# Performance work log

Hardware: AMD Instinct MI355X
Metric: run time of the kernel (lower is better)

Reference implementation:

```python
import jax, jax.numpy as jnp
import numpy as np

N_NODES = 50000
N_EDGES = 1600000
IN_CH = 128
HID_CH = 128


def setup_inputs() -> dict:
    key = jax.random.key(0)
    ks = jax.random.split(key, 8)
    node_embed = jax.random.normal(ks[0], (N_NODES, IN_CH), dtype=jnp.float32)
    node_pos = jax.random.normal(ks[1], (N_NODES, 3), dtype=jnp.float32)
    edge_index = jax.random.randint(ks[2], (2, N_EDGES), 0, N_NODES, dtype=jnp.int64)
    # Linear weights stored as [in, out] so y = x @ W + b (matches torch x @ W.T + b)
    W_res = jax.random.normal(ks[3], (IN_CH, HID_CH), dtype=jnp.float32) / np.sqrt(IN_CH)
    W_msg = jax.random.normal(ks[4], (2 * IN_CH + 1, HID_CH), dtype=jnp.float32) / np.sqrt(2 * IN_CH + 1)
    b_msg = jax.random.normal(ks[5], (HID_CH,), dtype=jnp.float32) * 0.01
    W_upd = jax.random.normal(ks[6], (IN_CH + HID_CH, HID_CH), dtype=jnp.float32) / np.sqrt(IN_CH + HID_CH)
    b_upd = jax.random.normal(ks[7], (HID_CH,), dtype=jnp.float32) * 0.01
    return {"node_embed": node_embed, "node_pos": node_pos, "edge_index": edge_index,
            "W_res": W_res, "W_msg": W_msg, "b_msg": b_msg, "W_upd": W_upd, "b_upd": b_upd}


def reference(node_embed, node_pos, edge_index, W_res, W_msg, b_msg, W_upd, b_upd):
    row, col = edge_index[0], edge_index[1]
    # squared distance per edge: [E, 1]
    diff = node_pos[row] - node_pos[col]
    dist = jnp.sum(diff * diff, axis=1, keepdims=True)
    # message MLP on concat(src, tgt, dist): [E, 2*in+1] -> [E, hidden]
    msg_in = jnp.concatenate([node_embed[row], node_embed[col], dist], axis=-1)
    msg = jax.nn.relu(msg_in @ W_msg + b_msg)
    # scatter-sum messages into target nodes (index = col, as in original)
    aggr = jax.ops.segment_sum(msg, col, num_segments=N_NODES)
    upd_in = jnp.concatenate([node_embed, aggr], axis=-1)
    new_node_embed = node_embed @ W_res + jax.nn.relu(upd_in @ W_upd + b_upd)
    return new_node_embed
```

## Files before the change

### kernel.cpp

```cpp
#include <hip/hip_runtime.h>
#include <hip/hip_bf16.h>
#include <cstdint>


typedef __bf16 bf16x8 __attribute__((ext_vector_type(8)));
typedef float floatx4 __attribute__((ext_vector_type(4)));
typedef float floatx2 __attribute__((ext_vector_type(2)));
typedef unsigned int uintx4 __attribute__((ext_vector_type(4)));

#define NBINS 1024
#define NCPY 8
#define BINF_CAP 384
#define CAP_OUT 2816
#define CUR_STRIDE 32
#define EPB 8192

__device__ __forceinline__ ushort f2bf(float f) {
  union { float f; uint i; } v; v.f = f;
  uint r = v.i + 0x7fff + ((v.i >> 16) & 1);
  return (ushort)(r >> 16);
}
__device__ __forceinline__ bf16x8 load_frag(const ushort* p) {
  uint4 v = *(const uint4*)p;
  return __builtin_bit_cast(bf16x8, v);
}
__device__ __forceinline__ floatx2 pmax0(floatx2 a) {
#if __has_builtin(__builtin_elementwise_max)
  return __builtin_elementwise_max(a, (floatx2)(0.f));
#else
  floatx2 r; r.x = fmaxf(a.x, 0.f); r.y = fmaxf(a.y, 0.f); return r;
#endif
}
__device__ __forceinline__ floatx2 cvtpk2(uint qu) {
#if __has_builtin(__builtin_amdgcn_cvt_pk_f32_fp8)
  return __builtin_amdgcn_cvt_pk_f32_fp8((int)qu, false);
#else
  floatx2 o = {__builtin_amdgcn_cvt_f32_fp8((int)qu, 0),
               __builtin_amdgcn_cvt_f32_fp8((int)qu, 1)};
  return o;
#endif
}

struct WSrc { const float* s[5]; };

__global__ __launch_bounds__(256) void k01_cast_bin(
    const float* __restrict__ embed, ushort* __restrict__ Eb, int n4, int nb_cast,
    WSrc ws, ushort* __restrict__ Wt,
    const int* __restrict__ ei, int E,
    uint* __restrict__ bin_cursor, uint* __restrict__ binned, int bb)
{
  __shared__ uint hist[NBINS];
  __shared__ uint sbase[NBINS];
  __shared__ uint lcur[NBINS];

  if ((int)blockIdx.x >= bb) {
    int cb = blockIdx.x - bb;
    if (cb < nb_cast) {
      int base = cb * 2048 + threadIdx.x;
#pragma unroll
      for (int k = 0; k < 8; ++k) {
        int i = base + k * 256;
        if (i < n4) {
          float4 v = ((const float4*)embed)[i];
          ushort4 o;
          o.x = f2bf(v.x); o.y = f2bf(v.y); o.z = f2bf(v.z); o.w = f2bf(v.w);
          ((ushort4*)Eb)[i] = o;
        }
      }
      return;
    }
    int wb = cb - nb_cast;
    const float* s = ws.s[wb];
    ushort* d = Wt + wb * 16384;
    for (int i = threadIdx.x; i < 16384; i += 256) {
      int k = i >> 7, n = i & 127;
      d[n * 128 + k] = f2bf(s[i]);
    }
    return;
  }

  const int t = threadIdx.x;
#pragma unroll
  for (int k = 0; k < NBINS / 256; ++k) hist[t + k * 256] = 0;
  __syncthreads();

  const int blk0 = blockIdx.x * EPB;
#pragma unroll
  for (int c = 0; c < EPB / 2048; ++c) {
    int e0 = blk0 + c * 2048 + t * 8;
    if (e0 < E) {
      int4 c0 = ((const int4*)(ei + E + e0))[0];
      int4 c1 = ((const int4*)(ei + E + e0))[1];
      int cc[8];
      cc[0]=c0.x; cc[1]=c0.y; cc[2]=c0.z; cc[3]=c0.w;
      cc[4]=c1.x; cc[5]=c1.y; cc[6]=c1.z; cc[7]=c1.w;
#pragma unroll
      for (int j = 0; j < 8; ++j)
        if (e0 + j < E) atomicAdd(&hist[cc[j] >> 6], 1u);
    }
  }
  __syncthreads();

  const int cpy = blockIdx.x & 7;
  uint* cur = bin_cursor + (size_t)cpy * NBINS * CUR_STRIDE;
#pragma unroll
  for (int k = 0; k < NBINS / 256; ++k) {
    int b2 = t + k * 256;
    uint h = hist[b2];
    sbase[b2] = h ? atomicAdd(cur + (size_t)b2 * CUR_STRIDE, h) : 0u;
    lcur[b2] = 0;
  }
  __syncthreads();

  uint* mybin = binned + (size_t)cpy * NBINS * BINF_CAP;
#pragma unroll
  for (int c = 0; c < EPB / 2048; ++c) {
    int e0 = blk0 + c * 2048 + t * 8;
    if (e0 < E) {
      int4 r0 = ((const int4*)(ei + e0))[0];
      int4 r1 = ((const int4*)(ei + e0))[1];
      int4 c0 = ((const int4*)(ei + E + e0))[0];
      int4 c1 = ((const int4*)(ei + E + e0))[1];
      int rr[8], cc[8];
      rr[0]=r0.x; rr[1]=r0.y; rr[2]=r0.z; rr[3]=r0.w;
      rr[4]=r1.x; rr[5]=r1.y; rr[6]=r1.z; rr[7]=r1.w;
      cc[0]=c0.x; cc[1]=c0.y; cc[2]=c0.z; cc[3]=c0.w;
      cc[4]=c1.x; cc[5]=c1.y; cc[6]=c1.z; cc[7]=c1.w;
#pragma unroll
      for (int j = 0; j < 8; ++j) {
        if (e0 + j < E) {
          int b = cc[j] >> 6;
          uint ofs = atomicAdd(&lcur[b], 1u);
          uint idx = sbase[b] + ofs;
          if (idx < BINF_CAP)
            mybin[(size_t)b * BINF_CAP + idx] = ((uint)cc[j] << 16) | (uint)rr[j];
        }
      }
    }
  }
}

__global__ __launch_bounds__(256) void k2_proj_sort(
    const ushort* __restrict__ Ab, int M, int rt,
    const ushort* __restrict__ W1t, const ushort* __restrict__ W2t,
    const float* __restrict__ b_msg, const float* __restrict__ pos,
    unsigned char* __restrict__ P1, ushort* __restrict__ P2b,
    const uint* __restrict__ bin_cursor, const uint* __restrict__ binned,
    uint* __restrict__ sorted, int* __restrict__ nstart, int* __restrict__ ncnt)
{
  __shared__ ushort sdist[NCPY * BINF_CAP];
  __shared__ uint   srt[CAP_OUT];
  __shared__ float  spos[64 * 3];
  __shared__ uint   h64[64], st64[64], lc64[64];
  __shared__ uint   ccnt[NCPY];
  __shared__ uint   stot;

  if ((int)blockIdx.x >= rt) {
    const int bin = blockIdx.x - rt;
    const int col0 = bin * 64;
    const int ncol = min(64, M - col0);
    const int tid = threadIdx.x;

    if (tid < 64) { h64[tid] = 0; lc64[tid] = 0; }
    if (tid < NCPY)
      ccnt[tid] = min(bin_cursor[((size_t)tid * NBINS + bin) * CUR_STRIDE],
                      (uint)BINF_CAP);
    for (int i = tid; i < ncol * 3; i += 256) spos[i] = pos[(size_t)col0 * 3 + i];
    __syncthreads();

    for (int c = 0; c < NCPY; ++c) {
      const int cnt = (int)ccnt[c];
      const uint* src = binned + ((size_t)c * NBINS + bin) * BINF_CAP;
      for (int i = tid; i < cnt; i += 256) {
        uint rc = src[i];
        uint row = rc & 0xffffu, c6 = (rc >> 16) & 63u;
        float dx = spos[c6 * 3 + 0] - pos[(size_t)row * 3 + 0];
        float dy = spos[c6 * 3 + 1] - pos[(size_t)row * 3 + 1];
        float dz = spos[c6 * 3 + 2] - pos[(size_t)row * 3 + 2];
        sdist[c * BINF_CAP + i] = f2bf(dx * dx + dy * dy + dz * dz);
        atomicAdd(&h64[c6], 1u);
      }
    }
    __syncthreads();

    if (tid == 0) {
      uint run = 0;
      for (int c = 0; c < 64; ++c) { st64[c] = run; run += (h64[c] + 3u) & ~3u; }
      stot = min(run, (uint)CAP_OUT);
    }
    __syncthreads();

    for (int c = 0; c < NCPY; ++c) {
      const int cnt = (int)ccnt[c];
      const uint* src = binned + ((size_t)c * NBINS + bin) * BINF_CAP;
      for (int i = tid; i < cnt; i += 256) {
        uint rc = src[i];
        uint c6 = (rc >> 16) & 63u;
        uint p = st64[c6] + atomicAdd(&lc64[c6], 1u);
        if (p < CAP_OUT)
          srt[p] = ((rc & 0xffffu) << 16) | (uint)sdist[c * BINF_CAP + i];
      }
    }
    __syncthreads();

    const size_t obase = (size_t)bin * CAP_OUT;
    for (int i = tid; i < (int)stot; i += 256)
      sorted[obase + i] = srt[i];
    if (tid < ncol) {
      nstart[col0 + tid] = (int)(obase + st64[tid]);
      ncnt[col0 + tid] = (int)h64[tid];
    }
    return;
  }

  const int wv = threadIdx.x >> 6, lane = threadIdx.x & 63;
  const int q = lane >> 4, lr = lane & 15;
  const int m0 = blockIdx.x * 32;
  const int n0 = wv * 32;

  const ushort* Wt2[2] = {W1t, W2t};
  bf16x8 bfr[2][2][4];
#pragma unroll
  for (int ws = 0; ws < 2; ++ws)
#pragma unroll
    for (int nt = 0; nt < 2; ++nt) {
      int colc = n0 + nt * 16 + lr;
#pragma unroll
      for (int kc = 0; kc < 4; ++kc)
        bfr[ws][nt][kc] = load_frag(Wt2[ws] + colc * 128 + kc * 32 + q * 8);
    }

  floatx4 z = {0.f, 0.f, 0.f, 0.f};
  floatx4 acc[2][2][2];
#pragma unroll
  for (int ws = 0; ws < 2; ++ws)
#pragma unroll
    for (int mt = 0; mt < 2; ++mt)
#pragma unroll
      for (int nt = 0; nt < 2; ++nt) acc[ws][mt][nt] = z;

  const int r0 = min(m0 + lr, M - 1);
  const int r1 = min(m0 + 16 + lr, M - 1);
#pragma unroll
  for (int kc = 0; kc < 4; ++kc) {
    bf16x8 a0 = load_frag(Ab + (size_t)r0 * 128 + kc * 32 + q * 8);
    bf16x8 a1 = load_frag(Ab + (size_t)r1 * 128 + kc * 32 + q * 8);
#pragma unroll
    for (int ws = 0; ws < 2; ++ws)
#pragma unroll
      for (int nt = 0; nt < 2; ++nt) {
        acc[ws][0][nt] = __builtin_amdgcn_mfma_f32_16x16x32_bf16(a0, bfr[ws][nt][kc], acc[ws][0][nt], 0, 0, 0);
        acc[ws][1][nt] = __builtin_amdgcn_mfma_f32_16x16x32_bf16(a1, bfr[ws][nt][kc], acc[ws][1][nt], 0, 0, 0);
      }
  }

#pragma unroll
  for (int nt = 0; nt < 2; ++nt) {
    int colc = n0 + nt * 16 + lr;
    float bias = b_msg[colc];
#pragma unroll
    for (int mt = 0; mt < 2; ++mt)
#pragma unroll
      for (int i = 0; i < 4; ++i) {
        int r = m0 + mt * 16 + q * 4 + i;
        if (r < M) {
          int p8 = __builtin_amdgcn_cvt_pk_fp8_f32(acc[0][mt][nt][i], 0.f, 0, false);
          P1[(size_t)r * 128 + colc] = (unsigned char)(p8 & 0xff);
          P2b[(size_t)r * 128 + colc] = f2bf(acc[1][mt][nt][i] + bias);
        }
      }
  }
}

__global__ __launch_bounds__(256) void aggregate(const int* __restrict__ ncnt,
                                                 const int* __restrict__ nstart,
                                                 const uint* __restrict__ sorted,
                                                 const unsigned char* __restrict__ P1,
                                                 const ushort* __restrict__ P2b,
                                                 const float* __restrict__ wd,
                                                 ushort* __restrict__ aggr, int M)
{
  const int lane = threadIdx.x & 63;
  const int ch = lane * 2;
  const int wid = blockIdx.x * 4 + (threadIdx.x >> 6);
  const int nw = gridDim.x * 4;

  float2 wl = *(const float2*)(wd + ch);
  floatx2 wv = {wl.x, wl.y};

  for (int n = wid; n < M; n += nw) {
    uint p2u = *(const uint*)(P2b + (size_t)n * 128 + ch);
    floatx2 p2 = {__int_as_float((int)(p2u << 16)),
                  __int_as_float((int)(p2u & 0xffff0000u))};

    const int cnt = ncnt[n];
    const uint* base = sorted + nstart[n];

    floatx2 accA = {0.f, 0.f}, accB = {0.f, 0.f};

    auto edge = [&](uint rec, floatx2& acc) {
      float d = __int_as_float((int)(rec << 16));
      uint off = ((rec >> 9) & 0x007fff80u) | (uint)ch;
      uint qu = (uint)*(const ushort*)(P1 + off);
#if __has_builtin(__builtin_elementwise_fma)
      floatx2 u = __builtin_elementwise_fma((floatx2)(d), wv, p2);
#else
      floatx2 u = (floatx2)(d) * wv + p2;
#endif
      floatx2 t = cvtpk2(qu) + u;
      acc += pmax0(t);
    };

    int i = 0;
    for (; i + 8 <= cnt; i += 8) {
      uintx4 ra = __builtin_nontemporal_load((const uintx4*)(base + i));
      uintx4 rb = __builtin_nontemporal_load((const uintx4*)(base + i + 4));
      edge(ra.x, accA); edge(ra.y, accB); edge(ra.z, accA); edge(ra.w, accB);
      edge(rb.x, accA); edge(rb.y, accB); edge(rb.z, accA); edge(rb.w, accB);
    }
    for (; i < cnt; ++i) edge(base[i], accA);

    floatx2 acc = accA + accB;
    uint o = (uint)f2bf(acc.x) | ((uint)f2bf(acc.y) << 16);
    *(uint*)(aggr + (size_t)n * 128 + ch) = o;
  }
}

__global__ __launch_bounds__(256) void gemm_upd_mfma(
    const ushort* __restrict__ Eb, const ushort* __restrict__ Gb, int M,
    const ushort* __restrict__ Wu1t, const ushort* __restrict__ Wu2t,
    const ushort* __restrict__ Wrt, const float* __restrict__ b_upd,
    float* __restrict__ out)
{
  const int wv = threadIdx.x >> 6, lane = threadIdx.x & 63;
  const int q = lane >> 4, lr = lane & 15;
  const int m0 = blockIdx.x * 32;
  const int n0 = wv * 32;

  bf16x8 b1[2][4], b2[2][4], br[2][4];
#pragma unroll
  for (int nt = 0; nt < 2; ++nt) {
    int colc = n0 + nt * 16 + lr;
#pragma unroll
    for (int kc = 0; kc < 4; ++kc) {
      b1[nt][kc] = load_frag(Wu1t + colc * 128 + kc * 32 + q * 8);
      b2[nt][kc] = load_frag(Wu2t + colc * 128 + kc * 32 + q * 8);
      br[nt][kc] = load_frag(Wrt  + colc * 128 + kc * 32 + q * 8);
    }
  }

  floatx4 z = {0.f, 0.f, 0.f, 0.f};
  floatx4 acc_u[2][2], acc_r[2][2];
#pragma unroll
  for (int mt = 0; mt < 2; ++mt)
#pragma unroll
    for (int nt = 0; nt < 2; ++nt) { acc_u[mt][nt] = z; acc_r[mt][nt] = z; }

  const int r0 = min(m0 + lr, M - 1);
  const int r1 = min(m0 + 16 + lr, M - 1);
#pragma unroll
  for (int kc = 0; kc < 4; ++kc) {
    bf16x8 ae0 = load_frag(Eb + (size_t)r0 * 128 + kc * 32 + q * 8);
    bf16x8 ae1 = load_frag(Eb + (size_t)r1 * 128 + kc * 32 + q * 8);
    bf16x8 ag0 = load_frag(Gb + (size_t)r0 * 128 + kc * 32 + q * 8);
    bf16x8 ag1 = load_frag(Gb + (size_t)r1 * 128 + kc * 32 + q * 8);
#pragma unroll
    for (int nt = 0; nt < 2; ++nt) {
      acc_u[0][nt] = __builtin_amdgcn_mfma_f32_16x16x32_bf16(ae0, b1[nt][kc], acc_u[0][nt], 0, 0, 0);
      acc_u[1][nt] = __builtin_amdgcn_mfma_f32_16x16x32_bf16(ae1, b1[nt][kc], acc_u[1][nt], 0, 0, 0);
      acc_u[0][nt] = __builtin_amdgcn_mfma_f32_16x16x32_bf16(ag0, b2[nt][kc], acc_u[0][nt], 0, 0, 0);
      acc_u[1][nt] = __builtin_amdgcn_mfma_f32_16x16x32_bf16(ag1, b2[nt][kc], acc_u[1][nt], 0, 0, 0);
      acc_r[0][nt] = __builtin_amdgcn_mfma_f32_16x16x32_bf16(ae0, br[nt][kc], acc_r[0][nt], 0, 0, 0);
      acc_r[1][nt] = __builtin_amdgcn_mfma_f32_16x16x32_bf16(ae1, br[nt][kc], acc_r[1][nt], 0, 0, 0);
    }
  }

#pragma unroll
  for (int nt = 0; nt < 2; ++nt) {
    int colc = n0 + nt * 16 + lr;
    float bias = b_upd[colc];
#pragma unroll
    for (int mt = 0; mt < 2; ++mt)
#pragma unroll
      for (int i = 0; i < 4; ++i) {
        int r = m0 + mt * 16 + q * 4 + i;
        if (r < M)
          out[(size_t)r * 128 + colc] = acc_r[mt][nt][i] + fmaxf(acc_u[mt][nt][i] + bias, 0.f);
      }
  }
}

extern "C" void kernel_launch(void* const* d_in, const int* in_sizes, int n_in,
                              void* d_out, int out_size, void* d_ws, size_t ws_size,
                              hipStream_t stream)
{
  const float* embed = (const float*)d_in[0];
  const float* pos   = (const float*)d_in[1];
  const int*   ei    = (const int*)d_in[2];
  const float* W_res = (const float*)d_in[3];
  const float* W_msg = (const float*)d_in[4];
  const float* b_msg = (const float*)d_in[5];
  const float* W_upd = (const float*)d_in[6];
  const float* b_upd = (const float*)d_in[7];
  float* out = (float*)d_out;

  const int M = in_sizes[0] / 128;
  const int E = in_sizes[2] / 2;

  ushort* Eb = (ushort*)d_ws;
  unsigned char* P1f8 = (unsigned char*)(Eb + (size_t)M * 128);
  ushort* P2b = (ushort*)(P1f8 + (size_t)M * 128);
  ushort* Gb  = P2b + (size_t)M * 128;
  ushort* Wt  = Gb  + (size_t)M * 128;
  uint*   binned = (uint*)(Wt + 5 * 16384);
  uint*   sorted = binned + (size_t)NCPY * NBINS * BINF_CAP;
  int*    nstart = (int*)(sorted + (size_t)NBINS * CAP_OUT);
  int*    ncnt   = nstart + M;
  uint*   bin_cursor = (uint*)(ncnt + M);

  (void)hipMemsetAsync(bin_cursor, 0,
                       (size_t)NCPY * NBINS * CUR_STRIDE * sizeof(uint), stream);

  WSrc wsrc;
  wsrc.s[0] = W_msg;
  wsrc.s[1] = W_msg + 128 * 128;
  wsrc.s[2] = W_res;
  wsrc.s[3] = W_upd;
  wsrc.s[4] = W_upd + 128 * 128;

  int n4 = M * 128 / 4;
  int nb_cast = (n4 + 2047) / 2048;
  int bb = (E + EPB - 1) / EPB;
  k01_cast_bin<<<bb + nb_cast + 5, 256, 0, stream>>>(
      embed, Eb, n4, nb_cast, wsrc, Wt, ei, E, bin_cursor, binned, bb);

  int rt = (M + 31) / 32;
  int nb2 = (M + 63) / 64;
  k2_proj_sort<<<rt + nb2, 256, 0, stream>>>(
      Eb, M, rt, Wt, Wt + 16384, b_msg, pos, P1f8, P2b,
      bin_cursor, binned, sorted, nstart, ncnt);

  int ab = min((M + 3) / 4, 2048);
  aggregate<<<ab, 256, 0, stream>>>(ncnt, nstart, sorted, P1f8, P2b,
                                    W_msg + 256 * 128, Gb, M);

  gemm_upd_mfma<<<rt, 256, 0, stream>>>(Eb, Gb, M, Wt + 3 * 16384, Wt + 4 * 16384,
                                        Wt + 2 * 16384, b_upd, out);
}
```

Measured before the change: 239.5 us.

## Split per-node edge lists by source half for P1 cache locality; restructure aggregate and upd GEMM

The sort stage now buckets each target's edges by whether the source row is in the lower or upper half of nodes and packs both counts into ncnt. The aggregate kernel processes a fixed set of 7 nodes per wave in two passes, first over low-half sources and then high-half sources, carrying partial sums in shared memory. The intent is to shrink the working set of P1 gathers per phase so they hit cache better. The update GEMM also processes four 32-row tiles per block to reuse the weight fragments held in registers. The risks are the extra shared-memory pass and reduced grid parallelism in the aggregate and GEMM kernels.

```diff
diff --git a/kernel.cpp b/kernel.cpp
--- a/kernel.cpp
+++ b/kernel.cpp
@@ -11,9 +11,10 @@
 #define NBINS 1024
 #define NCPY 8
 #define BINF_CAP 384
-#define CAP_OUT 2816
+#define CAP_OUT 3072
 #define CUR_STRIDE 32
 #define EPB 8192
+#define NPB 28
 
 __device__ __forceinline__ ushort f2bf(float f) {
   union { float f; uint i; } v; v.f = f;
@@ -151,7 +152,7 @@
   __shared__ ushort sdist[NCPY * BINF_CAP];
   __shared__ uint   srt[CAP_OUT];
   __shared__ float  spos[64 * 3];
-  __shared__ uint   h64[64], st64[64], lc64[64];
+  __shared__ uint   h128[128], st128[128], lc128[128];
   __shared__ uint   ccnt[NCPY];
   __shared__ uint   stot;
 
@@ -160,8 +161,9 @@
     const int col0 = bin * 64;
     const int ncol = min(64, M - col0);
     const int tid = threadIdx.x;
-
-    if (tid < 64) { h64[tid] = 0; lc64[tid] = 0; }
+    const uint halfM = (uint)(M >> 1);
+
+    if (tid < 128) { h128[tid] = 0; lc128[tid] = 0; }
     if (tid < NCPY)
       ccnt[tid] = min(bin_cursor[((size_t)tid * NBINS + bin) * CUR_STRIDE],
                       (uint)BINF_CAP);
@@ -178,14 +180,15 @@
         float dy = spos[c6 * 3 + 1] - pos[(size_t)row * 3 + 1];
         float dz = spos[c6 * 3 + 2] - pos[(size_t)row * 3 + 2];
         sdist[c * BINF_CAP + i] = f2bf(dx * dx + dy * dy + dz * dz);
-        atomicAdd(&h64[c6], 1u);
+        uint bk = (c6 << 1) | (row >= halfM ? 1u : 0u);
+        atomicAdd(&h128[bk], 1u);
       }
     }
     __syncthreads();
 
     if (tid == 0) {
       uint run = 0;
-      for (int c = 0; c < 64; ++c) { st64[c] = run; run += (h64[c] + 3u) & ~3u; }
+      for (int c = 0; c < 128; ++c) { st128[c] = run; run += (h128[c] + 3u) & ~3u; }
       stot = min(run, (uint)CAP_OUT);
     }
     __syncthreads();
@@ -195,10 +198,11 @@
       const uint* src = binned + ((size_t)c * NBINS + bin) * BINF_CAP;
       for (int i = tid; i < cnt; i += 256) {
         uint rc = src[i];
-        uint c6 = (rc >> 16) & 63u;
-        uint p = st64[c6] + atomicAdd(&lc64[c6], 1u);
+        uint row = rc & 0xffffu, c6 = (rc >> 16) & 63u;
+        uint bk = (c6 << 1) | (row >= halfM ? 1u : 0u);
+        uint p = st128[bk] + atomicAdd(&lc128[bk], 1u);
         if (p < CAP_OUT)
-          srt[p] = ((rc & 0xffffu) << 16) | (uint)sdist[c * BINF_CAP + i];
+          srt[p] = (row << 16) | (uint)sdist[c * BINF_CAP + i];
       }
     }
     __syncthreads();
@@ -207,8 +211,9 @@
     for (int i = tid; i < (int)stot; i += 256)
       sorted[obase + i] = srt[i];
     if (tid < ncol) {
-      nstart[col0 + tid] = (int)(obase + st64[tid]);
-      ncnt[col0 + tid] = (int)h64[tid];
+      uint lo = h128[2 * tid], hi = h128[2 * tid + 1];
+      nstart[col0 + tid] = (int)(obase + st128[2 * tid]);
+      ncnt[col0 + tid] = (int)(lo | (hi << 16));
     }
     return;
   }
@@ -280,50 +285,77 @@
                                                  const float* __restrict__ wd,
                                                  ushort* __restrict__ aggr, int M)
 {
+  __shared__ float2 accS[NPB][64];
+
   const int lane = threadIdx.x & 63;
   const int ch = lane * 2;
-  const int wid = blockIdx.x * 4 + (threadIdx.x >> 6);
-  const int nw = gridDim.x * 4;
+  const int w = threadIdx.x >> 6;
+  const int nbase = blockIdx.x * NPB + w * 7;
 
   float2 wl = *(const float2*)(wd + ch);
   floatx2 wv = {wl.x, wl.y};
 
-  for (int n = wid; n < M; n += nw) {
+#define EDGE_BODY(rec, acc)                                             \
+  {                                                                     \
+    float d = __int_as_float((int)((rec) << 16));                       \
+    uint off = (((rec) >> 9) & 0x007fff80u) | (uint)ch;                 \
+    uint qu = (uint)*(const ushort*)(P1 + off);                         \
+    floatx2 u = __builtin_elementwise_fma((floatx2)(d), wv, p2);        \
+    floatx2 tt = cvtpk2(qu) + u;                                        \
+    acc += pmax0(tt);                                                   \
+  }
+
+  for (int k = 0; k < 7; ++k) {
+    int n = nbase + k;
+    if (n >= M) break;
     uint p2u = *(const uint*)(P2b + (size_t)n * 128 + ch);
     floatx2 p2 = {__int_as_float((int)(p2u << 16)),
                   __int_as_float((int)(p2u & 0xffff0000u))};
-
-    const int cnt = ncnt[n];
+    const int cnt = ncnt[n] & 0xffff;
     const uint* base = sorted + nstart[n];
-
     floatx2 accA = {0.f, 0.f}, accB = {0.f, 0.f};
-
-    auto edge = [&](uint rec, floatx2& acc) {
-      float d = __int_as_float((int)(rec << 16));
-      uint off = ((rec >> 9) & 0x007fff80u) | (uint)ch;
-      uint qu = (uint)*(const ushort*)(P1 + off);
-#if __has_builtin(__builtin_elementwise_fma)
-      floatx2 u = __builtin_elementwise_fma((floatx2)(d), wv, p2);
-#else
-      floatx2 u = (floatx2)(d) * wv + p2;
-#endif
-      floatx2 t = cvtpk2(qu) + u;
-      acc += pmax0(t);
-    };
-
     int i = 0;
     for (; i + 8 <= cnt; i += 8) {
       uintx4 ra = __builtin_nontemporal_load((const uintx4*)(base + i));
       uintx4 rb = __builtin_nontemporal_load((const uintx4*)(base + i + 4));
-      edge(ra.x, accA); edge(ra.y, accB); edge(ra.z, accA); edge(ra.w, accB);
-      edge(rb.x, accA); edge(rb.y, accB); edge(rb.z, accA); edge(rb.w, accB);
-    }
-    for (; i < cnt; ++i) edge(base[i], accA);
-
+      EDGE_BODY(ra.x, accA) EDGE_BODY(ra.y, accB)
+      EDGE_BODY(ra.z, accA) EDGE_BODY(ra.w, accB)
+      EDGE_BODY(rb.x, accA) EDGE_BODY(rb.y, accB)
+      EDGE_BODY(rb.z, accA) EDGE_BODY(rb.w, accB)
+    }
+    for (; i < cnt; ++i) { uint rc = base[i]; EDGE_BODY(rc, accA) }
+    floatx2 acc = accA + accB;
+    accS[w * 7 + k][lane] = make_float2(acc.x, acc.y);
+  }
+
+
+  for (int k = 0; k < 7; ++k) {
+    int n = nbase + k;
+    if (n >= M) break;
+    uint p2u = *(const uint*)(P2b + (size_t)n * 128 + ch);
+    floatx2 p2 = {__int_as_float((int)(p2u << 16)),
+                  __int_as_float((int)(p2u & 0xffff0000u))};
+    uint pc = (uint)ncnt[n];
+    int clo = (int)(pc & 0xffffu);
+    int cnt = (int)(pc >> 16);
+    const uint* base = sorted + nstart[n] + ((clo + 3) & ~3);
+    float2 ls = accS[w * 7 + k][lane];
+    floatx2 accA = {ls.x, ls.y}, accB = {0.f, 0.f};
+    int i = 0;
+    for (; i + 8 <= cnt; i += 8) {
+      uintx4 ra = __builtin_nontemporal_load((const uintx4*)(base + i));
+      uintx4 rb = __builtin_nontemporal_load((const uintx4*)(base + i + 4));
+      EDGE_BODY(ra.x, accA) EDGE_BODY(ra.y, accB)
+      EDGE_BODY(ra.z, accA) EDGE_BODY(ra.w, accB)
+      EDGE_BODY(rb.x, accA) EDGE_BODY(rb.y, accB)
+      EDGE_BODY(rb.z, accA) EDGE_BODY(rb.w, accB)
+    }
+    for (; i < cnt; ++i) { uint rc = base[i]; EDGE_BODY(rc, accA) }
     floatx2 acc = accA + accB;
     uint o = (uint)f2bf(acc.x) | ((uint)f2bf(acc.y) << 16);
     *(uint*)(aggr + (size_t)n * 128 + ch) = o;
   }
+#undef EDGE_BODY
 }
 
 __global__ __launch_bounds__(256) void gemm_upd_mfma(
@@ -334,7 +366,7 @@
 {
   const int wv = threadIdx.x >> 6, lane = threadIdx.x & 63;
   const int q = lane >> 4, lr = lane & 15;
-  const int m0 = blockIdx.x * 32;
+  const int m0 = blockIdx.x * 128;
   const int n0 = wv * 32;
 
   bf16x8 b1[2][4], b2[2][4], br[2][4];
@@ -350,43 +382,49 @@
   }
 
   floatx4 z = {0.f, 0.f, 0.f, 0.f};
-  floatx4 acc_u[2][2], acc_r[2][2];
-#pragma unroll
-  for (int mt = 0; mt < 2; ++mt)
-#pragma unroll
-    for (int nt = 0; nt < 2; ++nt) { acc_u[mt][nt] = z; acc_r[mt][nt] = z; }
-
-  const int r0 = min(m0 + lr, M - 1);
-  const int r1 = min(m0 + 16 + lr, M - 1);
-#pragma unroll
-  for (int kc = 0; kc < 4; ++kc) {
-    bf16x8 ae0 = load_frag(Eb + (size_t)r0 * 128 + kc * 32 + q * 8);
-    bf16x8 ae1 = load_frag(Eb + (size_t)r1 * 128 + kc * 32 + q * 8);
-    bf16x8 ag0 = load_frag(Gb + (size_t)r0 * 128 + kc * 32 + q * 8);
-    bf16x8 ag1 = load_frag(Gb + (size_t)r1 * 128 + kc * 32 + q * 8);
+
+  for (int rc = 0; rc < 4; ++rc) {
+    const int mb = m0 + rc * 32;
+    if (mb >= M) break;
+
+    floatx4 acc_u[2][2], acc_r[2][2];
+#pragma unroll
+    for (int mt = 0; mt < 2; ++mt)
+#pragma unroll
+      for (int nt = 0; nt < 2; ++nt) { acc_u[mt][nt] = z; acc_r[mt][nt] = z; }
+
+    const int r0 = min(mb + lr, M - 1);
+    const int r1 = min(mb + 16 + lr, M - 1);
+#pragma unroll
+    for (int kc = 0; kc < 4; ++kc) {
+      bf16x8 ae0 = load_frag(Eb + (size_t)r0 * 128 + kc * 32 + q * 8);
+      bf16x8 ae1 = load_frag(Eb + (size_t)r1 * 128 + kc * 32 + q * 8);
+      bf16x8 ag0 = load_frag(Gb + (size_t)r0 * 128 + kc * 32 + q * 8);
+      bf16x8 ag1 = load_frag(Gb + (size_t)r1 * 128 + kc * 32 + q * 8);
+#pragma unroll
+      for (int nt = 0; nt < 2; ++nt) {
+        acc_u[0][nt] = __builtin_amdgcn_mfma_f32_16x16x32_bf16(ae0, b1[nt][kc], acc_u[0][nt], 0, 0, 0);
+        acc_u[1][nt] = __builtin_amdgcn_mfma_f32_16x16x32_bf16(ae1, b1[nt][kc], acc_u[1][nt], 0, 0, 0);
+        acc_u[0][nt] = __builtin_amdgcn_mfma_f32_16x16x32_bf16(ag0, b2[nt][kc], acc_u[0][nt], 0, 0, 0);
+        acc_u[1][nt] = __builtin_amdgcn_mfma_f32_16x16x32_bf16(ag1, b2[nt][kc], acc_u[1][nt], 0, 0, 0);
+        acc_r[0][nt] = __builtin_amdgcn_mfma_f32_16x16x32_bf16(ae0, br[nt][kc], acc_r[0][nt], 0, 0, 0);
+        acc_r[1][nt] = __builtin_amdgcn_mfma_f32_16x16x32_bf16(ae1, br[nt][kc], acc_r[1][nt], 0, 0, 0);
+      }
+    }
+
 #pragma unroll
     for (int nt = 0; nt < 2; ++nt) {
-      acc_u[0][nt] = __builtin_amdgcn_mfma_f32_16x16x32_bf16(ae0, b1[nt][kc], acc_u[0][nt], 0, 0, 0);
-      acc_u[1][nt] = __builtin_amdgcn_mfma_f32_16x16x32_bf16(ae1, b1[nt][kc], acc_u[1][nt], 0, 0, 0);
-      acc_u[0][nt] = __builtin_amdgcn_mfma_f32_16x16x32_bf16(ag0, b2[nt][kc], acc_u[0][nt], 0, 0, 0);
-      acc_u[1][nt] = __builtin_amdgcn_mfma_f32_16x16x32_bf16(ag1, b2[nt][kc], acc_u[1][nt], 0, 0, 0);
-      acc_r[0][nt] = __builtin_amdgcn_mfma_f32_16x16x32_bf16(ae0, br[nt][kc], acc_r[0][nt], 0, 0, 0);
-      acc_r[1][nt] = __builtin_amdgcn_mfma_f32_16x16x32_bf16(ae1, br[nt][kc], acc_r[1][nt], 0, 0, 0);
-    }
-  }
-
-#pragma unroll
-  for (int nt = 0; nt < 2; ++nt) {
-    int colc = n0 + nt * 16 + lr;
-    float bias = b_upd[colc];
-#pragma unroll
-    for (int mt = 0; mt < 2; ++mt)
-#pragma unroll
-      for (int i = 0; i < 4; ++i) {
-        int r = m0 + mt * 16 + q * 4 + i;
-        if (r < M)
-          out[(size_t)r * 128 + colc] = acc_r[mt][nt][i] + fmaxf(acc_u[mt][nt][i] + bias, 0.f);
-      }
+      int colc = n0 + nt * 16 + lr;
+      float bias = b_upd[colc];
+#pragma unroll
+      for (int mt = 0; mt < 2; ++mt)
+#pragma unroll
+        for (int i = 0; i < 4; ++i) {
+          int r = mb + mt * 16 + q * 4 + i;
+          if (r < M)
+            out[(size_t)r * 128 + colc] = acc_r[mt][nt][i] + fmaxf(acc_u[mt][nt][i] + bias, 0.f);
+        }
+    }
   }
 }
 
@@ -440,10 +478,11 @@
       Eb, M, rt, Wt, Wt + 16384, b_msg, pos, P1f8, P2b,
       bin_cursor, binned, sorted, nstart, ncnt);
 
-  int ab = min((M + 3) / 4, 2048);
+  int ab = (M + NPB - 1) / NPB;
   aggregate<<<ab, 256, 0, stream>>>(ncnt, nstart, sorted, P1f8, P2b,
                                     W_msg + 256 * 128, Gb, M);
 
-  gemm_upd_mfma<<<rt, 256, 0, stream>>>(Eb, Gb, M, Wt + 3 * 16384, Wt + 4 * 16384,
-                                        Wt + 2 * 16384, b_upd, out);
-}
+  int rt4 = (M + 127) / 128;
+  gemm_upd_mfma<<<rt4, 256, 0, stream>>>(Eb, Gb, M, Wt + 3 * 16384, Wt + 4 * 16384,
+                                         Wt + 2 * 16384, b_upd, out);
+}
```

Result: slower. 252.2 us (+5.3%).
